# Kernel tuning notes

Hardware: AMD Instinct MI355X
Metric: run time of the kernel (lower is better)

Reference implementation:

```python
import jax, jax.numpy as jnp
import numpy as np

B, S, IN, OUT, H, L, NH, STEPS = 256, 128, 64, 64, 1024, 2, 4, 16
HD = H // NH


def setup_inputs() -> dict:
    key = jax.random.key(0)
    ks = iter(jax.random.split(key, 32))
    std_h = 1.0 / np.sqrt(H)

    def u(k, shape, std):
        return jax.random.uniform(k, shape, jnp.float32, -std, std)

    inp = {"x": jax.random.normal(next(ks), (B, S, IN), jnp.float32)}
    # LSTM cells: stacked gate weights, gate order (i, f, g, o); y = x@Wx + h@Wh + b
    for name, din in (("e0", IN), ("e1", H), ("d0", OUT), ("d1", H)):
        inp[name + "_Wx"] = u(next(ks), (din, 4 * H), std_h)
        inp[name + "_Wh"] = u(next(ks), (H, 4 * H), std_h)
        inp[name + "_b"] = u(next(ks), (4 * H,), std_h)
    # attention linears (x@W + b convention)
    for name in ("Wq", "Wk", "Wv", "Wo"):
        inp[name] = u(next(ks), (H, H), std_h)
    for name in ("bq", "bk", "bv", "bo"):
        inp[name] = u(next(ks), (H,), std_h)
    inp["fc_W"] = u(next(ks), (2 * H, H), 1.0 / np.sqrt(2 * H))
    inp["fc_b"] = u(next(ks), (H,), 1.0 / np.sqrt(2 * H))
    inp["out_W"] = u(next(ks), (H, OUT), std_h)
    inp["out_b"] = u(next(ks), (OUT,), std_h)
    return inp


def _cell(x_t, h, c, Wx, Wh, b):
    z = x_t @ Wx + h @ Wh + b  # [B, 4H]
    i, f, g, o = jnp.split(z, 4, axis=-1)
    c = jax.nn.sigmoid(f) * c + jax.nn.sigmoid(i) * jnp.tanh(g)
    h = jax.nn.sigmoid(o) * jnp.tanh(c)
    return h, c


def _lstm_seq(x, Wx, Wh, b):
    # x: [B, T, D] -> outputs [B, T, H], final (h, c)
    h0 = jnp.zeros((x.shape[0], H), x.dtype)
    def step(carry, xt):
        h, c = carry
        h, c = _cell(xt, h, c, Wx, Wh, b)
        return (h, c), h
    (h, c), ys = jax.lax.scan(step, (h0, h0), jnp.swapaxes(x, 0, 1))
    return jnp.swapaxes(ys, 0, 1), h, c


def reference(x, e0_Wx, e0_Wh, e0_b, e1_Wx, e1_Wh, e1_b,
              d0_Wx, d0_Wh, d0_b, d1_Wx, d1_Wh, d1_b,
              Wq, bq, Wk, bk, Wv, bv, Wo, bo, fc_W, fc_b, out_W, out_b):
    # encoder: 2-layer manual LSTM (dropout=0, eval)
    y0, h0, c0 = _lstm_seq(x, e0_Wx, e0_Wh, e0_b)
    enc_out, h1, c1 = _lstm_seq(y0, e1_Wx, e1_Wh, e1_b)

    # K/V projections of encoder outputs (constant across decoder steps)
    Kp = (enc_out @ Wk + bk).reshape(B, S, NH, HD)
    Vp = (enc_out @ Wv + bv).reshape(B, S, NH, HD)
    scale = float(HD) ** 0.5

    def dstep(carry, _):
        dh0, dc0, dh1, dc1, xin = carry
        dh0, dc0 = _cell(xin, dh0, dc0, d0_Wx, d0_Wh, d0_b)
        dh1, dc1 = _cell(dh0, dh1, dc1, d1_Wx, d1_Wh, d1_b)
        q = (dh1 @ Wq + bq).reshape(B, NH, HD)
        scores = jnp.einsum('bnd,bsnd->bns', q, Kp) / scale
        w = jax.nn.softmax(scores, axis=-1)
        ctx = jnp.einsum('bns,bsnd->bnd', w, Vp).reshape(B, H)
        attn = ctx @ Wo + bo
        comb = jax.nn.relu(jnp.concatenate([dh1, attn], axis=-1) @ fc_W + fc_b)
        out = comb @ out_W + out_b  # [B, OUT]
        return (dh0, dc0, dh1, dc1, out), out

    init = (h0, c0, h1, c1, jnp.zeros((B, OUT), x.dtype))
    _, preds = jax.lax.scan(dstep, init, None, length=STEPS)
    return jnp.swapaxes(preds, 0, 1)  # [B, STEPS, OUT]
```

## Files before the change

kernel.cpp:

```cpp
#include <hip/hip_runtime.h>
#include <math.h>

typedef _Float16 h8 __attribute__((ext_vector_type(8)));
typedef _Float16 h4 __attribute__((ext_vector_type(4)));
typedef float f16v __attribute__((ext_vector_type(16)));

#define HPS 262144
#define XPS 2097152
#define IPS 16384

__device__ __forceinline__ float4 ld4(const float* p) { return *(const float4*)p; }
__device__ __forceinline__ float sigf(float x) { return 1.0f / (1.0f + expf(-x)); }
__device__ __forceinline__ float bf2f(unsigned short u) { return __uint_as_float(((unsigned)u) << 16); }
__device__ __forceinline__ float rdin(const void* p, size_t i, int bf) {
  return bf ? bf2f(((const unsigned short*)p)[i]) : ((const float*)p)[i];
}

__global__ void detect_dtype(const unsigned short* __restrict__ probe, int n, int* flag) {
  __shared__ int cnt;
  if (threadIdx.x == 0) cnt = 0;
  __syncthreads();
  int c = 0;
  for (int i = threadIdx.x; i < n; i += 256) {
    int e = (probe[i] >> 7) & 0xFF;
    if (e >= 100 && e <= 126) c++;
  }
  atomicAdd(&cnt, c);
  __syncthreads();
  if (threadIdx.x == 0) *flag = (cnt > (n * 3) / 4) ? 1 : 0;
}

__global__ void cvt_f32(const void* __restrict__ in, float* __restrict__ out, int n,
                        const int* __restrict__ flag) {
  int bf = *flag;
  int i = blockIdx.x * 256 + threadIdx.x;
  if (i < n) out[i] = rdin(in, i, bf);
}

__global__ void tsplit(const void* __restrict__ in, int N,
                       _Float16* __restrict__ outHi, _Float16* __restrict__ outLo,
                       int ldo, int kOff, int pOff, const int* __restrict__ flag) {
  __shared__ float tile[32][33];
  int bf = *flag;
  int kb = blockIdx.x * 32, nb = blockIdx.y * 32;
  for (int r = threadIdx.y; r < 32; r += 8)
    tile[threadIdx.x][r] = rdin(in, (size_t)(kb + r) * N + nb + threadIdx.x, bf);
  __syncthreads();
  for (int r = threadIdx.y; r < 32; r += 8) {
    float v = tile[r][threadIdx.x];
    _Float16 hi = (_Float16)v;
    _Float16 lo = (_Float16)(v - (float)hi);
    size_t o = (size_t)(pOff + nb + r) * ldo + kOff + kb + threadIdx.x;
    outHi[o] = hi; outLo[o] = lo;
  }
}

__global__ void f2h_kernel(const void* __restrict__ in, _Float16* __restrict__ out, int n,
                           const int* __restrict__ flag) {
  int bf = *flag;
  int i = blockIdx.x * 1024 + threadIdx.x * 4;
  if (i < n) {
    float vv[4];
#pragma unroll
    for (int k = 0; k < 4; ++k) vv[k] = rdin(in, i + k, bf);
    h4 hv, lv;
#pragma unroll
    for (int k = 0; k < 4; ++k) { hv[k] = (_Float16)vv[k]; lv[k] = (_Float16)(vv[k] - (float)hv[k]); }
    *(h4*)(out + i) = hv;
    *(h4*)(out + n + i) = lv;
  }
}

__global__ void sentinel_kernel(float* out, float v) { out[0] = v; }

__device__ __forceinline__ void gemm_tile(
    const _Float16* __restrict__ A0, int lda0, int aps0,
    const _Float16* __restrict__ A1, int lda1, int aps1, int ksplit,
    const _Float16* __restrict__ WTh, const _Float16* __restrict__ WTl, int ldw,
    int pbase, int c0, int c1, int mbase,
    float* __restrict__ zp, int zld, _Float16* Bs ) {
  const int tid = threadIdx.x;
  const int wv = tid >> 6, lane = tid & 63;
  const int l31 = lane & 31, lhi = lane >> 5;

  f16v acc00 = {}, acc01 = {}, acc10 = {}, acc11 = {};

  const int r0 = mbase + wv * 64 + l31;
  const int r1 = r0 + 32;
  const _Float16* a0b0 = A0 + (size_t)r0 * lda0;
  const _Float16* a1b0 = A1 + (size_t)r0 * lda1;
  const _Float16* a0b1 = A0 + (size_t)r1 * lda0;
  const _Float16* a1b1 = A1 + (size_t)r1 * lda1;

  const int spl = tid >> 7;
  const int sidx = tid & 127;
  const int sp = sidx >> 1;
  const int skh = (sidx & 1) << 4;
  const _Float16* srow = (spl ? WTl : WTh) + (size_t)(pbase + sp) * ldw + skh;
  _Float16* sdst = Bs + ((size_t)(spl * 64 + sp)) * 40 + skh;

  for (int c = c0; c < c1; ++c) {
    int k0 = c << 5;
    const _Float16* s = srow + k0;
    float4 v0 = *(const float4*)(s);
    float4 v1 = *(const float4*)(s + 8);
    __syncthreads();
    *(float4*)(sdst) = v0;
    *(float4*)(sdst + 8) = v1;
    __syncthreads();
#pragma unroll
    for (int sub = 0; sub < 2; ++sub) {
      int ks = k0 + sub * 16 + lhi * 8;
      const _Float16 *pa0, *pa1; int ap;
      if (ks < ksplit) { pa0 = a0b0 + ks; pa1 = a0b1 + ks; ap = aps0; }
      else { int kk = ks - ksplit; pa0 = a1b0 + kk; pa1 = a1b1 + kk; ap = aps1; }
      h8 af0h = *(const h8*)pa0;
      h8 af0l = *(const h8*)(pa0 + ap);
      h8 af1h = *(const h8*)pa1;
      h8 af1l = *(const h8*)(pa1 + ap);
      int kl = sub * 16 + lhi * 8;
      h8 b0h = *(const h8*)(Bs + (size_t)(l31) * 40 + kl);
      h8 b0l = *(const h8*)(Bs + (size_t)(64 + l31) * 40 + kl);
      h8 b1h = *(const h8*)(Bs + (size_t)(32 + l31) * 40 + kl);
      h8 b1l = *(const h8*)(Bs + (size_t)(96 + l31) * 40 + kl);
      acc00 = __builtin_amdgcn_mfma_f32_32x32x16_f16(af0h, b0h, acc00, 0, 0, 0);
      acc00 = __builtin_amdgcn_mfma_f32_32x32x16_f16(af0h, b0l, acc00, 0, 0, 0);
      acc00 = __builtin_amdgcn_mfma_f32_32x32x16_f16(af0l, b0h, acc00, 0, 0, 0);
      acc01 = __builtin_amdgcn_mfma_f32_32x32x16_f16(af0h, b1h, acc01, 0, 0, 0);
      acc01 = __builtin_amdgcn_mfma_f32_32x32x16_f16(af0h, b1l, acc01, 0, 0, 0);
      acc01 = __builtin_amdgcn_mfma_f32_32x32x16_f16(af0l, b1h, acc01, 0, 0, 0);
      acc10 = __builtin_amdgcn_mfma_f32_32x32x16_f16(af1h, b0h, acc10, 0, 0, 0);
      acc10 = __builtin_amdgcn_mfma_f32_32x32x16_f16(af1h, b0l, acc10, 0, 0, 0);
      acc10 = __builtin_amdgcn_mfma_f32_32x32x16_f16(af1l, b0h, acc10, 0, 0, 0);
      acc11 = __builtin_amdgcn_mfma_f32_32x32x16_f16(af1h, b1h, acc11, 0, 0, 0);
      acc11 = __builtin_amdgcn_mfma_f32_32x32x16_f16(af1h, b1l, acc11, 0, 0, 0);
      acc11 = __builtin_amdgcn_mfma_f32_32x32x16_f16(af1l, b1h, acc11, 0, 0, 0);
    }
  }

#pragma unroll
  for (int mi = 0; mi < 2; ++mi) {
#pragma unroll
    for (int ni = 0; ni < 2; ++ni) {
      f16v av = (mi == 0) ? (ni == 0 ? acc00 : acc01) : (ni == 0 ? acc10 : acc11);
      int col = pbase + ni * 32 + l31;
#pragma unroll
      for (int r = 0; r < 16; ++r) {
        int row = mbase + wv * 64 + mi * 32 + (r & 3) + ((r >> 2) * 8) + lhi * 4;
        zp[(size_t)row * zld + col] = av[r];
      }
    }
  }
}

__global__ __launch_bounds__(256) void enc_gemm(int t,
    const _Float16* xh, const _Float16* h0, const _Float16* h1,
    const _Float16* wt0h, const _Float16* wt0l,
    const _Float16* wt1h, const _Float16* wt1l,
    const _Float16* wtkvh, const _Float16* wtkvl,
    float* z0, float* z1, float* kvz) {
  __shared__ _Float16 Bs[2 * 64 * 40];
  int blk = blockIdx.x;
  if (blk < 128) {
    if (t > 127) return;
    int pg = blk & 63, kq = blk >> 6;
    gemm_tile(xh + (size_t)t * 64, 8192, XPS, h0, 1024, HPS, 64, wt0h, wt0l, 1088,
              pg * 64, kq * 17, kq * 17 + 17, 0, z0 + (size_t)kq * 1048576, 4096, Bs);
  } else if (blk < 256) {
    if (t < 1 || t > 128) return;
    int w = blk - 128, pg = w & 63, kq = w >> 6;
    gemm_tile(h0, 1024, HPS, h1, 1024, HPS, 1024, wt1h, wt1l, 2048,
              pg * 64, kq * 32, kq * 32 + 32, 0, z1 + (size_t)kq * 1048576, 4096, Bs);
  } else {
    if (t < 2) return;
    int w = blk - 256, pg = w & 31, kq = w >> 5;
    gemm_tile(h1, 1024, HPS, h1, 1024, HPS, 1024, wtkvh, wtkvl, 1024,
              pg * 64, kq * 16, kq * 16 + 16, 0, kvz + (size_t)kq * 524288, 2048, Bs);
  }
}

__global__ __launch_bounds__(256) void gemm_k(
    const _Float16* A0, int lda0, int aps0,
    const _Float16* A1, int lda1, int aps1, int ksplit,
    const _Float16* WTh, const _Float16* WTl, int ldw,
    int npg, int nkq, int tot, float* zp, int zld) {
  __shared__ _Float16 Bs[2 * 64 * 40];
  int pg = blockIdx.x % npg, kq = blockIdx.x / npg;
  int c0 = (tot * kq) / nkq, c1 = (tot * (kq + 1)) / nkq;
  gemm_tile(A0, lda0, aps0, A1, lda1, aps1, ksplit, WTh, WTl, ldw,
            pg * 64, c0, c1, 0, zp + (size_t)kq * 256 * zld, zld, Bs);
}

__device__ __forceinline__ void gates_body(const float* __restrict__ zp, int nparts,
    const float* __restrict__ bias, float* __restrict__ c,
    _Float16* __restrict__ h, int blk) {
  int e = blk * 1024 + threadIdx.x * 4;
  int b = e >> 10, j = e & 1023;
  size_t zrow = (size_t)b * 4096;
  float4 vi = ld4(bias + j), vf = ld4(bias + 1024 + j), vg = ld4(bias + 2048 + j), vo = ld4(bias + 3072 + j);
  for (int q = 0; q < nparts; ++q) {
    const float* zq = zp + (size_t)q * 1048576 + zrow;
    float4 t;
    t = ld4(zq + j);        vi.x += t.x; vi.y += t.y; vi.z += t.z; vi.w += t.w;
    t = ld4(zq + 1024 + j); vf.x += t.x; vf.y += t.y; vf.z += t.z; vf.w += t.w;
    t = ld4(zq + 2048 + j); vg.x += t.x; vg.y += t.y; vg.z += t.z; vg.w += t.w;
    t = ld4(zq + 3072 + j); vo.x += t.x; vo.y += t.y; vo.z += t.z; vo.w += t.w;
  }
  float* cp = c + (size_t)b * 1024 + j;
  float4 cv = ld4(cp);
  float zi[4] = {vi.x, vi.y, vi.z, vi.w}, zf[4] = {vf.x, vf.y, vf.z, vf.w};
  float zg[4] = {vg.x, vg.y, vg.z, vg.w}, zo[4] = {vo.x, vo.y, vo.z, vo.w};
  float cc[4] = {cv.x, cv.y, cv.z, cv.w};
  float hn[4];
#pragma unroll
  for (int k = 0; k < 4; ++k) {
    float ii = sigf(zi[k]), ff = sigf(zf[k]), gg = tanhf(zg[k]), oo = sigf(zo[k]);
    float cn = ff * cc[k] + ii * gg;
    cc[k] = cn;
    hn[k] = oo * tanhf(cn);
  }
  float4 co; co.x = cc[0]; co.y = cc[1]; co.z = cc[2]; co.w = cc[3];
  *(float4*)cp = co;
  h4 hv, lv;
#pragma unroll
  for (int k = 0; k < 4; ++k) { hv[k] = (_Float16)hn[k]; lv[k] = (_Float16)(hn[k] - (float)hv[k]); }
  *(h4*)(h + (size_t)b * 1024 + j) = hv;
  *(h4*)(h + HPS + (size_t)b * 1024 + j) = lv;
}

__global__ void enc_gates(int t, const float* z0, const float* z1, const float* kvz,
                          const float* b0, const float* b1,
                          const float* bk, const float* bv,
                          float* c0, float* c1, _Float16* h0, _Float16* h1,
                          _Float16* Kp, _Float16* Vp) {
  int blk = blockIdx.x;
  if (blk < 256) {
    if (t > 127) return;
    gates_body(z0, 2, b0, c0, h0, blk);
  } else if (blk < 512) {
    if (t < 1 || t > 128) return;
    gates_body(z1, 2, b1, c1, h1, blk - 256);
  } else {
    if (t < 2) return;
    int e = (blk - 512) * 1024 + threadIdx.x * 4;
    int b = e >> 11, col = e & 2047;
    const float* bb = (col < 1024) ? (bk + col) : (bv + col - 1024);
    float4 v = ld4(bb);
    for (int q = 0; q < 2; ++q) {
      float4 tt = ld4(kvz + (size_t)q * 524288 + e);
      v.x += tt.x; v.y += tt.y; v.z += tt.z; v.w += tt.w;
    }
    _Float16* dst = (col < 1024) ? Kp : Vp;
    int cc = (col < 1024) ? col : col - 1024;
    h4 hv; hv[0] = (_Float16)v.x; hv[1] = (_Float16)v.y; hv[2] = (_Float16)v.z; hv[3] = (_Float16)v.w;
    *(h4*)(dst + (size_t)(b * 128 + (t - 2)) * 1024 + cc) = hv;
  }
}

__global__ void dec_gates(const float* zp, int nparts, const float* bias,
                          float* c, _Float16* h) {
  gates_body(zp, nparts, bias, c, h, blockIdx.x);
}

__global__ void reduce_act(const float* __restrict__ zp, int nparts,
                           const float* __restrict__ bias, _Float16* __restrict__ out, int relu) {
  int e = blockIdx.x * 1024 + threadIdx.x * 4;
  int j = e & 1023;
  float4 v = ld4(bias + j);
  for (int q = 0; q < nparts; ++q) {
    float4 t = ld4(zp + (size_t)q * 262144 + e);
    v.x += t.x; v.y += t.y; v.z += t.z; v.w += t.w;
  }
  if (relu) {
    v.x = fmaxf(v.x, 0.f); v.y = fmaxf(v.y, 0.f); v.z = fmaxf(v.z, 0.f); v.w = fmaxf(v.w, 0.f);
  }
  float vv[4] = {v.x, v.y, v.z, v.w};
  h4 hv, lv;
#pragma unroll
  for (int k = 0; k < 4; ++k) { hv[k] = (_Float16)vv[k]; lv[k] = (_Float16)(vv[k] - (float)hv[k]); }
  *(h4*)(out + e) = hv;
  *(h4*)(out + HPS + e) = lv;
}

__global__ void out_reduce(const float* __restrict__ op, const float* __restrict__ outb,
                           float* __restrict__ dout, _Float16* __restrict__ xin, int s) {
  int e = blockIdx.x * 1024 + threadIdx.x * 4;
  int b = e >> 6, o = e & 63;
  float4 v = ld4(outb + o);
  for (int q = 0; q < 16; ++q) {
    float4 t = ld4(op + (size_t)q * 16384 + e);
    v.x += t.x; v.y += t.y; v.z += t.z; v.w += t.w;
  }
  *(float4*)(dout + (size_t)(b * 16 + s) * 64 + o) = v;
  float vv[4] = {v.x, v.y, v.z, v.w};
  h4 hv, lv;
#pragma unroll
  for (int k = 0; k < 4; ++k) { hv[k] = (_Float16)vv[k]; lv[k] = (_Float16)(vv[k] - (float)hv[k]); }
  *(h4*)(xin + e) = hv;
  *(h4*)(xin + IPS + e) = lv;
}

__global__ void attn_kernel(const float* __restrict__ qp, const float* __restrict__ bq,
                            const _Float16* __restrict__ Kp, const _Float16* __restrict__ Vp,
                            _Float16* __restrict__ ctx) {
  int b = blockIdx.x >> 2, n = blockIdx.x & 3;
  __shared__ float qs[256];
  __shared__ float sw[128];
  int tid = threadIdx.x;
  float qv = bq[n * 256 + tid];
  for (int q = 0; q < 4; ++q) qv += qp[(size_t)q * 262144 + (size_t)b * 1024 + n * 256 + tid];
  qs[tid] = qv;
  __syncthreads();
  int w = tid >> 6, lane = tid & 63;
  for (int s = w; s < 128; s += 4) {
    const _Float16* kr = Kp + (size_t)(b * 128 + s) * 1024 + n * 256;
    float acc = 0.f;
#pragma unroll
    for (int d = 0; d < 4; ++d) acc += qs[lane + d * 64] * (float)kr[lane + d * 64];
    for (int off = 32; off; off >>= 1) acc += __shfl_down(acc, off);
    if (lane == 0) sw[s] = acc * 0.0625f;
  }
  __syncthreads();
  if (w == 0) {
    float a = sw[lane], bb = sw[lane + 64];
    float m = fmaxf(a, bb);
    for (int off = 32; off; off >>= 1) m = fmaxf(m, __shfl_down(m, off));
    m = __shfl(m, 0);
    float e1 = expf(a - m), e2 = expf(bb - m);
    float ss = e1 + e2;
    for (int off = 32; off; off >>= 1) ss += __shfl_down(ss, off);
    ss = __shfl(ss, 0);
    float inv = 1.0f / ss;
    sw[lane] = e1 * inv; sw[lane + 64] = e2 * inv;
  }
  __syncthreads();
  float acc = 0.f;
  const _Float16* vb = Vp + (size_t)b * 131072 + n * 256 + tid;
  for (int s2 = 0; s2 < 128; ++s2) acc += sw[s2] * (float)vb[(size_t)s2 * 1024];
  size_t idx = (size_t)b * 1024 + n * 256 + tid;
  _Float16 hi = (_Float16)acc;
  ctx[idx] = hi;
  ctx[HPS + idx] = (_Float16)(acc - (float)hi);
}

extern "C" void kernel_launch(void* const* d_in, const int* in_sizes, int n_in,
                              void* d_out, int out_size, void* d_ws, size_t ws_size,
                              hipStream_t stream) {
  const void* x     = d_in[0];
  const void* e0_Wx = d_in[1];
  const void* e0_Wh = d_in[2];
  const void* e0_b  = d_in[3];
  const void* e1_Wx = d_in[4];
  const void* e1_Wh = d_in[5];
  const void* e1_b  = d_in[6];
  const void* d0_Wx = d_in[7];
  const void* d0_Wh = d_in[8];
  const void* d0_b  = d_in[9];
  const void* d1_Wx = d_in[10];
  const void* d1_Wh = d_in[11];
  const void* d1_b  = d_in[12];
  const void* Wq = d_in[13];
  const void* Wk = d_in[14];
  const void* Wv = d_in[15];
  const void* Wo = d_in[16];
  const void* bq = d_in[17];
  const void* bk = d_in[18];
  const void* bv = d_in[19];
  const void* bo = d_in[20];
  const void* fc_W  = d_in[21];
  const void* fc_b  = d_in[22];
  const void* out_W = d_in[23];
  const void* out_b = d_in[24];

  char* p = (char*)d_ws;
  auto alloc = [&](size_t bytes) { char* r = p; p += (bytes + 255) & ~(size_t)255; return r; };

  int* flag = (int*)alloc(256);
  float* bias_arena = (float*)alloc(87040);
  float* c_e0b = bias_arena +     0;
  float* c_e1b = bias_arena +  4096;
  float* c_d0b = bias_arena +  8192;
  float* c_d1b = bias_arena + 12288;
  float* c_bq  = bias_arena + 16384;
  float* c_bk  = bias_arena + 17408;
  float* c_bv  = bias_arena + 18432;
  float* c_bo  = bias_arena + 19456;
  float* c_fcb = bias_arena + 20480;
  float* c_ob  = bias_arena + 21504;

  char* warena = alloc(68419584);
  _Float16* wt_e0h = (_Float16*)(warena);
  _Float16* wt_e0l = (_Float16*)(warena +  8912896);
  _Float16* wt_e1h = (_Float16*)(warena + 17825792);
  _Float16* wt_e1l = (_Float16*)(warena + 34603008);
  _Float16* wt_kvh = (_Float16*)(warena + 51380224);
  _Float16* wt_kvl = (_Float16*)(warena + 55574528);
  _Float16* xh     = (_Float16*)(warena + 59768832);
  _Float16* wt_d0h = (_Float16*)(warena);
  _Float16* wt_d0l = (_Float16*)(warena +  8912896);
  _Float16* wt_d1h = (_Float16*)(warena + 17825792);
  _Float16* wt_d1l = (_Float16*)(warena + 34603008);
  _Float16* wt_qh  = (_Float16*)(warena + 51380224);
  _Float16* wt_ql  = (_Float16*)(warena + 53477376);
  _Float16* wt_oh  = (_Float16*)(warena + 55574528);
  _Float16* wt_ol  = (_Float16*)(warena + 57671680);
  _Float16* wt_fch = (_Float16*)(warena + 59768832);
  _Float16* wt_fcl = (_Float16*)(warena + 63963136);
  _Float16* wt_outh= (_Float16*)(warena + 68157440);
  _Float16* wt_outl= (_Float16*)(warena + 68288512);

  char* zero0 = p;
  _Float16* h0 = (_Float16*)alloc(1048576);
  _Float16* h1 = (_Float16*)alloc(1048576);
  float* c0 = (float*)alloc(1048576);
  float* c1 = (float*)alloc(1048576);
  _Float16* xin = (_Float16*)alloc(65536);
  size_t zeroBytes = (size_t)(p - zero0);
  _Float16* Kp = (_Float16*)alloc(67108864);
  _Float16* Vp = (_Float16*)alloc(67108864);
  float* zarena = (float*)alloc(20971520);
  float* z0e = zarena;
  float* z1e = zarena + 2097152;
  float* kvz = zarena + 4194304;
  float* zdec = zarena;
  float* fcp = zarena;
  float* qp  = zarena + 2097152;
  float* op  = zarena + 3145728;
  _Float16* ctx    = (_Float16*)alloc(1048576);
  _Float16* attn_h = (_Float16*)alloc(1048576);
  _Float16* comb   = (_Float16*)alloc(1048576);

  if ((size_t)(p - (char*)d_ws) > ws_size) {
    sentinel_kernel<<<1, 1, 0, stream>>>((float*)d_out, 1.0e9f + (float)ws_size);
    return;
  }

  detect_dtype<<<1, 256, 0, stream>>>((const unsigned short*)e0_Wx, 16384, flag);
  cvt_f32<<<16, 256, 0, stream>>>(e0_b, c_e0b, 4096, flag);
  cvt_f32<<<16, 256, 0, stream>>>(e1_b, c_e1b, 4096, flag);
  cvt_f32<<<16, 256, 0, stream>>>(d0_b, c_d0b, 4096, flag);
  cvt_f32<<<16, 256, 0, stream>>>(d1_b, c_d1b, 4096, flag);
  cvt_f32<<<4, 256, 0, stream>>>(bq, c_bq, 1024, flag);
  cvt_f32<<<4, 256, 0, stream>>>(bk, c_bk, 1024, flag);
  cvt_f32<<<4, 256, 0, stream>>>(bv, c_bv, 1024, flag);
  cvt_f32<<<4, 256, 0, stream>>>(bo, c_bo, 1024, flag);
  cvt_f32<<<4, 256, 0, stream>>>(fc_b, c_fcb, 1024, flag);
  cvt_f32<<<1, 64, 0, stream>>>(out_b, c_ob, 64, flag);

  dim3 tb(32, 8);
  tsplit<<<dim3(2, 128), tb, 0, stream>>>(e0_Wx, 4096, wt_e0h, wt_e0l, 1088, 0, 0, flag);
  tsplit<<<dim3(32, 128), tb, 0, stream>>>(e0_Wh, 4096, wt_e0h, wt_e0l, 1088, 64, 0, flag);
  tsplit<<<dim3(32, 128), tb, 0, stream>>>(e1_Wx, 4096, wt_e1h, wt_e1l, 2048, 0, 0, flag);
  tsplit<<<dim3(32, 128), tb, 0, stream>>>(e1_Wh, 4096, wt_e1h, wt_e1l, 2048, 1024, 0, flag);
  tsplit<<<dim3(32, 32), tb, 0, stream>>>(Wk, 1024, wt_kvh, wt_kvl, 1024, 0, 0, flag);
  tsplit<<<dim3(32, 32), tb, 0, stream>>>(Wv, 1024, wt_kvh, wt_kvl, 1024, 0, 1024, flag);
  f2h_kernel<<<2048, 256, 0, stream>>>(x, xh, 2097152, flag);
  hipMemsetAsync(zero0, 0, zeroBytes, stream);

  for (int t = 0; t <= 129; ++t) {
    enc_gemm<<<320, 256, 0, stream>>>(t, xh, h0, h1, wt_e0h, wt_e0l, wt_e1h, wt_e1l,
                                      wt_kvh, wt_kvl, z0e, z1e, kvz);
    enc_gates<<<1024, 256, 0, stream>>>(t, z0e, z1e, kvz, c_e0b, c_e1b, c_bk, c_bv,
                                        c0, c1, h0, h1, Kp, Vp);
  }

  tsplit<<<dim3(2, 128), tb, 0, stream>>>(d0_Wx, 4096, wt_d0h, wt_d0l, 1088, 0, 0, flag);
  tsplit<<<dim3(32, 128), tb, 0, stream>>>(d0_Wh, 4096, wt_d0h, wt_d0l, 1088, 64, 0, flag);
  tsplit<<<dim3(32, 128), tb, 0, stream>>>(d1_Wx, 4096, wt_d1h, wt_d1l, 2048, 0, 0, flag);
  tsplit<<<dim3(32, 128), tb, 0, stream>>>(d1_Wh, 4096, wt_d1h, wt_d1l, 2048, 1024, 0, flag);
  tsplit<<<dim3(32, 32), tb, 0, stream>>>(Wq, 1024, wt_qh, wt_ql, 1024, 0, 0, flag);
  tsplit<<<dim3(32, 32), tb, 0, stream>>>(Wo, 1024, wt_oh, wt_ol, 1024, 0, 0, flag);
  tsplit<<<dim3(64, 32), tb, 0, stream>>>(fc_W, 1024, wt_fch, wt_fcl, 2048, 0, 0, flag);
  tsplit<<<dim3(32, 2), tb, 0, stream>>>(out_W, 64, wt_outh, wt_outl, 1024, 0, 0, flag);

  for (int s = 0; s < 16; ++s) {
    gemm_k<<<256, 256, 0, stream>>>(xin, 64, IPS, h0, 1024, HPS, 64,
                                    wt_d0h, wt_d0l, 1088, 64, 4, 34, zdec, 4096);
    dec_gates<<<256, 256, 0, stream>>>(zdec, 4, c_d0b, c0, h0);
    gemm_k<<<256, 256, 0, stream>>>(h0, 1024, HPS, h1, 1024, HPS, 1024,
                                    wt_d1h, wt_d1l, 2048, 64, 4, 64, zdec, 4096);
    dec_gates<<<256, 256, 0, stream>>>(zdec, 4, c_d1b, c1, h1);
    gemm_k<<<64, 256, 0, stream>>>(h1, 1024, HPS, h1, 1024, HPS, 1024,
                                   wt_qh, wt_ql, 1024, 16, 4, 32, qp, 1024);
    attn_kernel<<<1024, 256, 0, stream>>>(qp, c_bq, Kp, Vp, ctx);
    gemm_k<<<64, 256, 0, stream>>>(ctx, 1024, HPS, ctx, 1024, HPS, 1024,
                                   wt_oh, wt_ol, 1024, 16, 4, 32, qp, 1024);
    reduce_act<<<256, 256, 0, stream>>>(qp, 4, c_bo, attn_h, 0);
    gemm_k<<<128, 256, 0, stream>>>(h1, 1024, HPS, attn_h, 1024, HPS, 1024,
                                    wt_fch, wt_fcl, 2048, 16, 8, 64, fcp, 1024);
    reduce_act<<<256, 256, 0, stream>>>(fcp, 8, c_fcb, comb, 1);
    gemm_k<<<16, 256, 0, stream>>>(comb, 1024, HPS, comb, 1024, HPS, 1024,
                                   wt_outh, wt_outl, 1024, 1, 16, 32, op, 64);
    out_reduce<<<16, 256, 0, stream>>>(op, c_ob, (float*)d_out, xin, s);
  }
}
```

Measured before the change: 10.45 ms.

## Double-buffer GEMM weight tiles, widen encoder split-K, fuse q and fc-h1 GEMMs

The GEMM tile loop now double-buffers the shared-memory weight tile, prefetching the next K-chunk while MFMAs run, which removes one barrier per iteration. The encoder layer-1 GEMM is split into four K-parts when workspace allows, falling back to two, so more blocks are launched. In the decoder, the Wq projection and the h1 half of the fc GEMM are merged into one kernel, and the later fc launch covers only the attention half. Launch bounds request two blocks per CU. The cost is more LDS, larger partial-sum buffers and more reduction work in the gates kernel.

```diff
diff --git a/kernel.cpp b/kernel.cpp
--- a/kernel.cpp
+++ b/kernel.cpp
@@ -8,6 +8,8 @@
 #define HPS 262144
 #define XPS 2097152
 #define IPS 16384
+#define BSTR 40
+#define BUFE (128 * BSTR)
 
 __device__ __forceinline__ float4 ld4(const float* p) { return *(const float4*)p; }
 __device__ __forceinline__ float sigf(float x) { return 1.0f / (1.0f + expf(-x)); }
@@ -77,7 +79,7 @@
     const _Float16* __restrict__ A0, int lda0, int aps0,
     const _Float16* __restrict__ A1, int lda1, int aps1, int ksplit,
     const _Float16* __restrict__ WTh, const _Float16* __restrict__ WTl, int ldw,
-    int pbase, int c0, int c1, int mbase,
+    int pbase, int c0, int c1,
     float* __restrict__ zp, int zld, _Float16* Bs ) {
   const int tid = threadIdx.x;
   const int wv = tid >> 6, lane = tid & 63;
@@ -85,7 +87,7 @@
 
   f16v acc00 = {}, acc01 = {}, acc10 = {}, acc11 = {};
 
-  const int r0 = mbase + wv * 64 + l31;
+  const int r0 = wv * 64 + l31;
   const int r1 = r0 + 32;
   const _Float16* a0b0 = A0 + (size_t)r0 * lda0;
   const _Float16* a1b0 = A1 + (size_t)r0 * lda1;
@@ -97,17 +99,29 @@
   const int sp = sidx >> 1;
   const int skh = (sidx & 1) << 4;
   const _Float16* srow = (spl ? WTl : WTh) + (size_t)(pbase + sp) * ldw + skh;
-  _Float16* sdst = Bs + ((size_t)(spl * 64 + sp)) * 40 + skh;
-
-  for (int c = c0; c < c1; ++c) {
-    int k0 = c << 5;
-    const _Float16* s = srow + k0;
+  const int sdoff = (spl * 64 + sp) * BSTR + skh;
+
+  {
+    const _Float16* s = srow + (c0 << 5);
     float4 v0 = *(const float4*)(s);
     float4 v1 = *(const float4*)(s + 8);
+    _Float16* d = Bs + sdoff;
+    *(float4*)(d) = v0;
+    *(float4*)(d + 8) = v1;
+  }
+
+  int buf = 0;
+  for (int c = c0; c < c1; ++c) {
     __syncthreads();
-    *(float4*)(sdst) = v0;
-    *(float4*)(sdst + 8) = v1;
-    __syncthreads();
+    float4 n0, n1;
+    const bool more = (c + 1 < c1);
+    if (more) {
+      const _Float16* s = srow + ((c + 1) << 5);
+      n0 = *(const float4*)(s);
+      n1 = *(const float4*)(s + 8);
+    }
+    const _Float16* bb = Bs + buf * BUFE;
+    int k0 = c << 5;
 #pragma unroll
     for (int sub = 0; sub < 2; ++sub) {
       int ks = k0 + sub * 16 + lhi * 8;
@@ -119,10 +133,10 @@
       h8 af1h = *(const h8*)pa1;
       h8 af1l = *(const h8*)(pa1 + ap);
       int kl = sub * 16 + lhi * 8;
-      h8 b0h = *(const h8*)(Bs + (size_t)(l31) * 40 + kl);
-      h8 b0l = *(const h8*)(Bs + (size_t)(64 + l31) * 40 + kl);
-      h8 b1h = *(const h8*)(Bs + (size_t)(32 + l31) * 40 + kl);
-      h8 b1l = *(const h8*)(Bs + (size_t)(96 + l31) * 40 + kl);
+      h8 b0h = *(const h8*)(bb + (size_t)(l31) * BSTR + kl);
+      h8 b0l = *(const h8*)(bb + (size_t)(64 + l31) * BSTR + kl);
+      h8 b1h = *(const h8*)(bb + (size_t)(32 + l31) * BSTR + kl);
+      h8 b1l = *(const h8*)(bb + (size_t)(96 + l31) * BSTR + kl);
       acc00 = __builtin_amdgcn_mfma_f32_32x32x16_f16(af0h, b0h, acc00, 0, 0, 0);
       acc00 = __builtin_amdgcn_mfma_f32_32x32x16_f16(af0h, b0l, acc00, 0, 0, 0);
       acc00 = __builtin_amdgcn_mfma_f32_32x32x16_f16(af0l, b0h, acc00, 0, 0, 0);
@@ -136,6 +150,12 @@
       acc11 = __builtin_amdgcn_mfma_f32_32x32x16_f16(af1h, b1l, acc11, 0, 0, 0);
       acc11 = __builtin_amdgcn_mfma_f32_32x32x16_f16(af1l, b1h, acc11, 0, 0, 0);
     }
+    if (more) {
+      _Float16* d = Bs + (buf ^ 1) * BUFE + sdoff;
+      *(float4*)(d) = n0;
+      *(float4*)(d + 8) = n1;
+    }
+    buf ^= 1;
   }
 
 #pragma unroll
@@ -146,49 +166,69 @@
       int col = pbase + ni * 32 + l31;
 #pragma unroll
       for (int r = 0; r < 16; ++r) {
-        int row = mbase + wv * 64 + mi * 32 + (r & 3) + ((r >> 2) * 8) + lhi * 4;
+        int row = wv * 64 + mi * 32 + (r & 3) + ((r >> 2) * 8) + lhi * 4;
         zp[(size_t)row * zld + col] = av[r];
       }
     }
   }
 }
 
-__global__ __launch_bounds__(256) void enc_gemm(int t,
+__global__ __launch_bounds__(256, 2) void enc_gemm(int t, int l1kq,
     const _Float16* xh, const _Float16* h0, const _Float16* h1,
     const _Float16* wt0h, const _Float16* wt0l,
     const _Float16* wt1h, const _Float16* wt1l,
     const _Float16* wtkvh, const _Float16* wtkvl,
     float* z0, float* z1, float* kvz) {
-  __shared__ _Float16 Bs[2 * 64 * 40];
+  __shared__ _Float16 Bs[2 * BUFE];
   int blk = blockIdx.x;
-  if (blk < 128) {
+  int nl1 = 64 * l1kq;
+  if (blk < nl1) {
+    if (t < 1 || t > 128) return;
+    int pg = blk & 63, kq = blk >> 6;
+    int c0 = (64 * kq) / l1kq, c1 = (64 * (kq + 1)) / l1kq;
+    gemm_tile(h0, 1024, HPS, h1, 1024, HPS, 1024, wt1h, wt1l, 2048,
+              pg * 64, c0, c1, z1 + (size_t)kq * 1048576, 4096, Bs);
+  } else if (blk < nl1 + 128) {
     if (t > 127) return;
-    int pg = blk & 63, kq = blk >> 6;
+    int w = blk - nl1, pg = w & 63, kq = w >> 6;
     gemm_tile(xh + (size_t)t * 64, 8192, XPS, h0, 1024, HPS, 64, wt0h, wt0l, 1088,
-              pg * 64, kq * 17, kq * 17 + 17, 0, z0 + (size_t)kq * 1048576, 4096, Bs);
-  } else if (blk < 256) {
-    if (t < 1 || t > 128) return;
-    int w = blk - 128, pg = w & 63, kq = w >> 6;
-    gemm_tile(h0, 1024, HPS, h1, 1024, HPS, 1024, wt1h, wt1l, 2048,
-              pg * 64, kq * 32, kq * 32 + 32, 0, z1 + (size_t)kq * 1048576, 4096, Bs);
+              pg * 64, kq * 17, kq * 17 + 17, z0 + (size_t)kq * 1048576, 4096, Bs);
   } else {
     if (t < 2) return;
-    int w = blk - 256, pg = w & 31, kq = w >> 5;
+    int w = blk - nl1 - 128, pg = w & 31, kq = w >> 5;
     gemm_tile(h1, 1024, HPS, h1, 1024, HPS, 1024, wtkvh, wtkvl, 1024,
-              pg * 64, kq * 16, kq * 16 + 16, 0, kvz + (size_t)kq * 524288, 2048, Bs);
-  }
-}
-
-__global__ __launch_bounds__(256) void gemm_k(
+              pg * 64, kq * 16, kq * 16 + 16, kvz + (size_t)kq * 524288, 2048, Bs);
+  }
+}
+
+__global__ __launch_bounds__(256, 2) void gemm_k(
     const _Float16* A0, int lda0, int aps0,
     const _Float16* A1, int lda1, int aps1, int ksplit,
     const _Float16* WTh, const _Float16* WTl, int ldw,
-    int npg, int nkq, int tot, float* zp, int zld) {
-  __shared__ _Float16 Bs[2 * 64 * 40];
-  int pg = blockIdx.x % npg, kq = blockIdx.x / npg;
+    int npg, int nkq, int tot, int kqoff, float* zp, int zld) {
+  __shared__ _Float16 Bs[2 * BUFE];
+  int pg = blockIdx.x % npg, kq = blockIdx.x / npg + kqoff;
   int c0 = (tot * kq) / nkq, c1 = (tot * (kq + 1)) / nkq;
   gemm_tile(A0, lda0, aps0, A1, lda1, aps1, ksplit, WTh, WTl, ldw,
-            pg * 64, c0, c1, 0, zp + (size_t)kq * 256 * zld, zld, Bs);
+            pg * 64, c0, c1, zp + (size_t)kq * 256 * zld, zld, Bs);
+}
+
+__global__ __launch_bounds__(256, 2) void qfc_kernel(
+    const _Float16* h1,
+    const _Float16* wqh, const _Float16* wql,
+    const _Float16* wfh, const _Float16* wfl,
+    float* qp, float* fcp) {
+  __shared__ _Float16 Bs[2 * BUFE];
+  int blk = blockIdx.x;
+  if (blk < 64) {
+    int pg = blk & 15, kq = blk >> 4;
+    gemm_tile(h1, 1024, HPS, h1, 1024, HPS, 1024, wqh, wql, 1024,
+              pg * 64, kq * 8, kq * 8 + 8, qp + (size_t)kq * 262144, 1024, Bs);
+  } else {
+    int w = blk - 64, pg = w & 15, kq = w >> 4;
+    gemm_tile(h1, 1024, HPS, h1, 1024, HPS, 1024, wfh, wfl, 2048,
+              pg * 64, kq * 8, kq * 8 + 8, fcp + (size_t)kq * 262144, 1024, Bs);
+  }
 }
 
 __device__ __forceinline__ void gates_body(const float* __restrict__ zp, int nparts,
@@ -228,7 +268,7 @@
   *(h4*)(h + HPS + (size_t)b * 1024 + j) = lv;
 }
 
-__global__ void enc_gates(int t, const float* z0, const float* z1, const float* kvz,
+__global__ void enc_gates(int t, int l1parts, const float* z0, const float* z1, const float* kvz,
                           const float* b0, const float* b1,
                           const float* bk, const float* bv,
                           float* c0, float* c1, _Float16* h0, _Float16* h1,
@@ -239,7 +279,7 @@
     gates_body(z0, 2, b0, c0, h0, blk);
   } else if (blk < 512) {
     if (t < 1 || t > 128) return;
-    gates_body(z1, 2, b1, c1, h1, blk - 256);
+    gates_body(z1, l1parts, b1, c1, h1, blk - 256);
   } else {
     if (t < 2) return;
     int e = (blk - 512) * 1024 + threadIdx.x * 4;
@@ -372,11 +412,40 @@
   const void* out_W = d_in[23];
   const void* out_b = d_in[24];
 
+  int l1parts = 4;
   char* p = (char*)d_ws;
-  auto alloc = [&](size_t bytes) { char* r = p; p += (bytes + 255) & ~(size_t)255; return r; };
-
-  int* flag = (int*)alloc(256);
-  float* bias_arena = (float*)alloc(87040);
+  int* flag; float* bias_arena; char* warena; char* zero0;
+  _Float16 *h0, *h1, *xin, *Kp, *Vp, *ctx, *attn_h, *comb;
+  float *c0, *c1; float* zarena;
+  size_t zeroBytes = 0;
+
+  for (int attempt = 0; attempt < 2; ++attempt) {
+    p = (char*)d_ws;
+    auto alloc = [&](size_t bytes) { char* r = p; p += (bytes + 255) & ~(size_t)255; return r; };
+    flag = (int*)alloc(256);
+    bias_arena = (float*)alloc(87040);
+    warena = alloc(68419584);
+    zero0 = p;
+    h0 = (_Float16*)alloc(1048576);
+    h1 = (_Float16*)alloc(1048576);
+    c0 = (float*)alloc(1048576);
+    c1 = (float*)alloc(1048576);
+    xin = (_Float16*)alloc(65536);
+    zeroBytes = (size_t)(p - zero0);
+    Kp = (_Float16*)alloc(67108864);
+    Vp = (_Float16*)alloc(67108864);
+    zarena = (float*)alloc((size_t)(3 + l1parts) * 4194304);
+    ctx    = (_Float16*)alloc(1048576);
+    attn_h = (_Float16*)alloc(1048576);
+    comb   = (_Float16*)alloc(1048576);
+    if ((size_t)(p - (char*)d_ws) <= ws_size) break;
+    l1parts = 2;
+  }
+  if ((size_t)(p - (char*)d_ws) > ws_size) {
+    sentinel_kernel<<<1, 1, 0, stream>>>((float*)d_out, 1.0e9f + (float)ws_size);
+    return;
+  }
+
   float* c_e0b = bias_arena +     0;
   float* c_e1b = bias_arena +  4096;
   float* c_d0b = bias_arena +  8192;
@@ -388,7 +457,6 @@
   float* c_fcb = bias_arena + 20480;
   float* c_ob  = bias_arena + 21504;
 
-  char* warena = alloc(68419584);
   _Float16* wt_e0h = (_Float16*)(warena);
   _Float16* wt_e0l = (_Float16*)(warena +  8912896);
   _Float16* wt_e1h = (_Float16*)(warena + 17825792);
@@ -409,31 +477,13 @@
   _Float16* wt_outh= (_Float16*)(warena + 68157440);
   _Float16* wt_outl= (_Float16*)(warena + 68288512);
 
-  char* zero0 = p;
-  _Float16* h0 = (_Float16*)alloc(1048576);
-  _Float16* h1 = (_Float16*)alloc(1048576);
-  float* c0 = (float*)alloc(1048576);
-  float* c1 = (float*)alloc(1048576);
-  _Float16* xin = (_Float16*)alloc(65536);
-  size_t zeroBytes = (size_t)(p - zero0);
-  _Float16* Kp = (_Float16*)alloc(67108864);
-  _Float16* Vp = (_Float16*)alloc(67108864);
-  float* zarena = (float*)alloc(20971520);
   float* z0e = zarena;
   float* z1e = zarena + 2097152;
-  float* kvz = zarena + 4194304;
+  float* kvz = z1e + (size_t)l1parts * 1048576;
   float* zdec = zarena;
   float* fcp = zarena;
   float* qp  = zarena + 2097152;
   float* op  = zarena + 3145728;
-  _Float16* ctx    = (_Float16*)alloc(1048576);
-  _Float16* attn_h = (_Float16*)alloc(1048576);
-  _Float16* comb   = (_Float16*)alloc(1048576);
-
-  if ((size_t)(p - (char*)d_ws) > ws_size) {
-    sentinel_kernel<<<1, 1, 0, stream>>>((float*)d_out, 1.0e9f + (float)ws_size);
-    return;
-  }
 
   detect_dtype<<<1, 256, 0, stream>>>((const unsigned short*)e0_Wx, 16384, flag);
   cvt_f32<<<16, 256, 0, stream>>>(e0_b, c_e0b, 4096, flag);
@@ -457,10 +507,12 @@
   f2h_kernel<<<2048, 256, 0, stream>>>(x, xh, 2097152, flag);
   hipMemsetAsync(zero0, 0, zeroBytes, stream);
 
+  int encBlocks = 64 * l1parts + 192;
   for (int t = 0; t <= 129; ++t) {
-    enc_gemm<<<320, 256, 0, stream>>>(t, xh, h0, h1, wt_e0h, wt_e0l, wt_e1h, wt_e1l,
-                                      wt_kvh, wt_kvl, z0e, z1e, kvz);
-    enc_gates<<<1024, 256, 0, stream>>>(t, z0e, z1e, kvz, c_e0b, c_e1b, c_bk, c_bv,
+    enc_gemm<<<encBlocks, 256, 0, stream>>>(t, l1parts, xh, h0, h1,
+                                            wt_e0h, wt_e0l, wt_e1h, wt_e1l,
+                                            wt_kvh, wt_kvl, z0e, z1e, kvz);
+    enc_gates<<<1024, 256, 0, stream>>>(t, l1parts, z0e, z1e, kvz, c_e0b, c_e1b, c_bk, c_bv,
                                         c0, c1, h0, h1, Kp, Vp);
   }
 
@@ -475,22 +527,21 @@
 
   for (int s = 0; s < 16; ++s) {
     gemm_k<<<256, 256, 0, stream>>>(xin, 64, IPS, h0, 1024, HPS, 64,
-                                    wt_d0h, wt_d0l, 1088, 64, 4, 34, zdec, 4096);
+                                    wt_d0h, wt_d0l, 1088, 64, 4, 34, 0, zdec, 4096);
     dec_gates<<<256, 256, 0, stream>>>(zdec, 4, c_d0b, c0, h0);
     gemm_k<<<256, 256, 0, stream>>>(h0, 1024, HPS, h1, 1024, HPS, 1024,
-                                    wt_d1h, wt_d1l, 2048, 64, 4, 64, zdec, 4096);
+                                    wt_d1h, wt_d1l, 2048, 64, 4, 64, 0, zdec, 4096);
     dec_gates<<<256, 256, 0, stream>>>(zdec, 4, c_d1b, c1, h1);
-    gemm_k<<<64, 256, 0, stream>>>(h1, 1024, HPS, h1, 1024, HPS, 1024,
-                                   wt_qh, wt_ql, 1024, 16, 4, 32, qp, 1024);
+    qfc_kernel<<<128, 256, 0, stream>>>(h1, wt_qh, wt_ql, wt_fch, wt_fcl, qp, fcp);
     attn_kernel<<<1024, 256, 0, stream>>>(qp, c_bq, Kp, Vp, ctx);
     gemm_k<<<64, 256, 0, stream>>>(ctx, 1024, HPS, ctx, 1024, HPS, 1024,
-                                   wt_oh, wt_ol, 1024, 16, 4, 32, qp, 1024);
+                                   wt_oh, wt_ol, 1024, 16, 4, 32, 0, qp, 1024);
     reduce_act<<<256, 256, 0, stream>>>(qp, 4, c_bo, attn_h, 0);
-    gemm_k<<<128, 256, 0, stream>>>(h1, 1024, HPS, attn_h, 1024, HPS, 1024,
-                                    wt_fch, wt_fcl, 2048, 16, 8, 64, fcp, 1024);
+    gemm_k<<<64, 256, 0, stream>>>(h1, 1024, HPS, attn_h, 1024, HPS, 1024,
+                                   wt_fch, wt_fcl, 2048, 16, 8, 64, 4, fcp, 1024);
     reduce_act<<<256, 256, 0, stream>>>(fcp, 8, c_fcb, comb, 1);
     gemm_k<<<16, 256, 0, stream>>>(comb, 1024, HPS, comb, 1024, HPS, 1024,
-                                   wt_outh, wt_outl, 1024, 1, 16, 32, op, 64);
+                                   wt_outh, wt_outl, 1024, 1, 16, 32, 0, op, 64);
     out_reduce<<<16, 256, 0, stream>>>(op, c_ob, (float*)d_out, xin, s);
   }
 }
```

New measurement: 9.562 ms. 1.09x faster.
